# Optimization experiments

Hardware: AMD Instinct MI355X
Metric: run time of the kernel (lower is better)

## Reference

```python
import jax, jax.numpy as jnp
import numpy as np

D_MODEL = 1024
NUM_HEADS = 16
MAX_LEN = 512  # chunk_size
BATCH = 2
SEQ_LEN = 2048


def _mha(x, w_in, b_in, w_out, b_out, num_heads):
    """torch.nn.MultiheadAttention (eval mode, self-attn) over the last-but-one axis.
    x: (..., S, d). Packed in-proj weight w_in: (3d, d), out-proj w_out: (d, d)."""
    *batch, S, d = x.shape
    hd = d // num_heads
    qkv = x @ w_in.T + b_in                      # (..., S, 3d)
    q, k, v = jnp.split(qkv, 3, axis=-1)
    def heads(t):
        return t.reshape(*batch, S, num_heads, hd)
    q, k, v = heads(q), heads(k), heads(v)
    scale = 1.0 / np.sqrt(hd).astype(np.float32)
    scores = jnp.einsum('...qhd,...khd->...hqk', q, k) * scale
    attn = jax.nn.softmax(scores, axis=-1)
    o = jnp.einsum('...hqk,...khd->...qhd', attn, v).reshape(*batch, S, d)
    return o @ w_out.T + b_out


def setup_inputs() -> dict:
    key = jax.random.key(0)
    ks = jax.random.split(key, 5)
    d = D_MODEL
    s = 0.02
    return {
        'x': jax.random.normal(ks[0], (BATCH, SEQ_LEN, d), dtype=jnp.float32),
        'w_in_l': jax.random.normal(ks[1], (3 * d, d), dtype=jnp.float32) * s,
        'b_in_l': jnp.zeros((3 * d,), jnp.float32),
        'w_out_l': jax.random.normal(ks[2], (d, d), dtype=jnp.float32) * s,
        'b_out_l': jnp.zeros((d,), jnp.float32),
        'w_in_g': jax.random.normal(ks[3], (3 * d, d), dtype=jnp.float32) * s,
        'b_in_g': jnp.zeros((3 * d,), jnp.float32),
        'w_out_g': jax.random.normal(ks[4], (d, d), dtype=jnp.float32) * s,
        'b_out_g': jnp.zeros((d,), jnp.float32),
    }


def reference(x, w_in_l, b_in_l, w_out_l, b_out_l, w_in_g, b_in_g, w_out_g, b_out_g):
    B, S, d = x.shape
    cs = MAX_LEN
    nc = S // cs
    # (B, nc, cs, d) -> (B, cs, nc, d): for each intra-chunk position, attend across chunks.
    xc = x.reshape(B, nc, cs, d).transpose(0, 2, 1, 3)
    # Vectorized replacement for the python loop over chunk positions:
    # batched MHA with batch (B, cs) and sequence length nc.
    loc = _mha(xc, w_in_l, b_in_l, w_out_l, b_out_l, NUM_HEADS)  # (B, cs, nc, d)
    # Faithful to torch: stack -> (nc, cs, B, d), transpose(1,2) -> (nc, B, cs, d),
    # then raw reshape to (B, S, d) (a layout-reinterpreting view, preserved here).
    loc = loc.transpose(2, 0, 1, 3).reshape(B, S, d)
    # Global full self-attention over the whole sequence.
    return _mha(loc, w_in_g, b_in_g, w_out_g, b_out_g, NUM_HEADS)
```

## Files before the change

kernel.cpp:

```cpp
#include <hip/hip_runtime.h>

#define BB 2
#define SS 2048
#define DD 1024
#define HH 16
#define HD 64
#define CS 512
#define NC 4
#define TD 3072
#define MM 4096

typedef __attribute__((ext_vector_type(8))) short short8;
typedef __attribute__((ext_vector_type(4))) float floatx4;

__device__ __forceinline__ float bf2f(unsigned short h) {
  union { unsigned int u; float f; } v; v.u = ((unsigned int)h) << 16; return v.f;
}
__device__ __forceinline__ unsigned short f2bf(float f) {
  union { float f; unsigned int u; } v; v.f = f;
  unsigned int r = (v.u + 0x7fffu + ((v.u >> 16) & 1u)) >> 16;
  return (unsigned short)r;
}
__device__ __forceinline__ short8 ld8f(const float* p) {
  floatx4 f0 = *(const floatx4*)p;
  floatx4 f1 = *(const floatx4*)(p + 4);
  short8 o;
  o[0] = (short)f2bf(f0[0]); o[1] = (short)f2bf(f0[1]);
  o[2] = (short)f2bf(f0[2]); o[3] = (short)f2bf(f0[3]);
  o[4] = (short)f2bf(f1[0]); o[5] = (short)f2bf(f1[1]);
  o[6] = (short)f2bf(f1[2]); o[7] = (short)f2bf(f1[3]);
  return o;
}
__device__ __forceinline__ short8 scale8_eighth(short8 a) {
  short8 o;
#pragma unroll
  for (int j = 0; j < 8; ++j) o[j] = (short)f2bf(bf2f((unsigned short)a[j]) * 0.125f);
  return o;
}
__device__ __forceinline__ void async16(const void* g, void* l) {
  __builtin_amdgcn_global_load_lds((const __attribute__((address_space(1))) void*)g,
                                   (__attribute__((address_space(3))) void*)l, 16, 0, 0);
}

__global__ __launch_bounds__(256) void cvt_bf16(const float* __restrict__ in,
                                                unsigned short* __restrict__ out, int n) {
  int i = (blockIdx.x * 256 + threadIdx.x) * 8;
  if (i < n) *(short8*)(out + i) = ld8f(in + i);
}

template <int W_F32, int C_F32>
__global__ __launch_bounds__(256) void gemm_bt_bias(
    const unsigned short* __restrict__ A, const void* __restrict__ Wv,
    const float* __restrict__ bias, void* __restrict__ Cv, int M, int N, int K) {
  __shared__ unsigned short sA[128 * 32];
  __shared__ unsigned short sB[128 * 32];
  const int tid = threadIdx.x;
  const int wid = tid >> 6, lane = tid & 63;
  const int quad = lane >> 4, l15 = lane & 15;
  const int wm = wid & 1, wn = wid >> 1;
  const int bm = blockIdx.y, bn = blockIdx.x;

  floatx4 acc[4][4];
#pragma unroll
  for (int i = 0; i < 4; ++i)
#pragma unroll
    for (int j = 0; j < 4; ++j) acc[i][j] = (floatx4){0.f, 0.f, 0.f, 0.f};

  const int r = tid >> 2;
  const int kc = (tid & 3) * 8;
  const unsigned short* gA = A + (size_t)(bm * 128 + r) * K + kc;
  const float*          gWf = (const float*)Wv          + (size_t)(bn * 128 + r) * K + kc;
  const unsigned short* gWh = (const unsigned short*)Wv + (size_t)(bn * 128 + r) * K + kc;
  unsigned short* lA = sA + wid * 512;
  unsigned short* lB = sB + wid * 512;

  for (int k0 = 0; k0 < K; k0 += 32) {
    async16(gA + k0, lA);
    async16(gA + (size_t)64 * K + k0, lA + 2048);
    if (W_F32) {
      short8 b0 = ld8f(gWf + k0);
      short8 b1 = ld8f(gWf + (size_t)64 * K + k0);
      *(short8*)(sB + r * 32 + kc) = b0;
      *(short8*)(sB + (64 + r) * 32 + kc) = b1;
    } else {
      async16(gWh + k0, lB);
      async16(gWh + (size_t)64 * K + k0, lB + 2048);
    }
    __syncthreads();

    short8 af[4], bfr[4];
#pragma unroll
    for (int i = 0; i < 4; ++i)
      af[i] = *(const short8*)(sA + (wm * 64 + i * 16 + l15) * 32 + quad * 8);
#pragma unroll
    for (int j = 0; j < 4; ++j)
      bfr[j] = *(const short8*)(sB + (wn * 64 + j * 16 + l15) * 32 + quad * 8);
#pragma unroll
    for (int i = 0; i < 4; ++i)
#pragma unroll
      for (int j = 0; j < 4; ++j)
        acc[i][j] = __builtin_amdgcn_mfma_f32_16x16x32_bf16(af[i], bfr[j], acc[i][j], 0, 0, 0);
    __syncthreads();
  }

#pragma unroll
  for (int j = 0; j < 4; ++j) {
    int n = bn * 128 + wn * 64 + j * 16 + l15;
    float bv = bias[n];
#pragma unroll
    for (int i = 0; i < 4; ++i) {
      int mrow = bm * 128 + wm * 64 + i * 16 + quad * 4;
#pragma unroll
      for (int rr = 0; rr < 4; ++rr) {
        float v = acc[i][j][rr] + bv;
        if (C_F32) ((float*)Cv)[(size_t)(mrow + rr) * N + n] = v;
        else ((unsigned short*)Cv)[(size_t)(mrow + rr) * N + n] = f2bf(v);
      }
    }
  }
}

__global__ __launch_bounds__(256) void attn_local(const unsigned short* __restrict__ QKV,
                                                  unsigned short* __restrict__ O) {
  const int tid = threadIdx.x;
  const int wid = tid >> 6, lane = tid & 63;
  const int idx = blockIdx.x * 4 + wid;
  const int h = idx & 15, c = (idx >> 4) & 511, b = idx >> 13;

  float q[NC], k[NC], v[NC];
#pragma unroll
  for (int n = 0; n < NC; ++n) {
    size_t base = (size_t)(b * SS + n * CS + c) * TD + h * HD + lane;
    q[n] = bf2f(QKV[base]);
    k[n] = bf2f(QKV[base + DD]);
    v[n] = bf2f(QKV[base + 2 * DD]);
  }
  float s[NC][NC];
#pragma unroll
  for (int m = 0; m < NC; ++m)
#pragma unroll
    for (int n = 0; n < NC; ++n) {
      float p = q[m] * k[n];
#pragma unroll
      for (int off = 32; off >= 1; off >>= 1) p += __shfl_xor(p, off);
      s[m][n] = p * 0.125f;
    }
#pragma unroll
  for (int m = 0; m < NC; ++m) {
    float mx = fmaxf(fmaxf(s[m][0], s[m][1]), fmaxf(s[m][2], s[m][3]));
    float e[NC], sum = 0.f;
#pragma unroll
    for (int n = 0; n < NC; ++n) { e[n] = __expf(s[m][n] - mx); sum += e[n]; }
    float o = (e[0] * v[0] + e[1] * v[1] + e[2] * v[2] + e[3] * v[3]) / sum;
    O[(size_t)(m * (BB * CS) + b * CS + c) * DD + h * HD + lane] = f2bf(o);
  }
}

__global__ __launch_bounds__(256) void transpose_v(const unsigned short* __restrict__ QKV,
                                                   unsigned short* __restrict__ VT) {
  __shared__ unsigned short sT[64 * 64];
  const int tid = threadIdx.x;
  const int bh = blockIdx.x, b = bh >> 4, h = bh & 15;
  const int s0 = blockIdx.y * 64;
#pragma unroll
  for (int it = 0; it < 2; ++it) {
    int C = it * 256 + tid;
    int t = C >> 3, dc = C & 7;
    short8 v = *(const short8*)(QKV + (size_t)(b * SS + s0 + t) * TD + 2 * DD + h * HD + dc * 8);
    *(short8*)(sT + t * 64 + ((dc ^ (t & 7)) << 3)) = v;
  }
  __syncthreads();
#pragma unroll
  for (int it = 0; it < 2; ++it) {
    int C = it * 256 + tid;
    int d = C >> 3, tc = C & 7;
    short8 o;
#pragma unroll
    for (int j = 0; j < 8; ++j) {
      int t = tc * 8 + j;
      o[j] = (short)sT[t * 64 + (((d >> 3) ^ (t & 7)) << 3) + (d & 7)];
    }
    *(short8*)(VT + ((size_t)(bh * 64 + d)) * SS + s0 + tc * 8) = o;
  }
}

__global__ __launch_bounds__(256) void attn_global(
    const unsigned short* __restrict__ Q, const unsigned short* __restrict__ K,
    const unsigned short* __restrict__ VT, unsigned short* __restrict__ O) {
  __shared__ unsigned short sK[64 * 64];
  __shared__ unsigned short sVT[64 * 64];
  __shared__ unsigned short sP[4][16 * 64];
  const int tid = threadIdx.x;
  const int wid = tid >> 6, lane = tid & 63;
  const int quad = lane >> 4, l15 = lane & 15;
  const int bh = blockIdx.x;
  const int b = bh >> 4, h = bh & 15;
  const int q0 = blockIdx.y * 64 + wid * 16;

  const unsigned short* qrow = Q + (size_t)(b * SS + q0 + l15) * TD + h * HD + quad * 8;
  const short8 qf0 = scale8_eighth(*(const short8*)(qrow));
  const short8 qf1 = scale8_eighth(*(const short8*)(qrow + 32));

  float lsum[4] = {0.f, 0.f, 0.f, 0.f};
  floatx4 oacc[4];
#pragma unroll
  for (int s = 0; s < 4; ++s) oacc[s] = (floatx4){0.f, 0.f, 0.f, 0.f};

  unsigned short* myP = &sP[wid][0];

  for (int kt = 0; kt < SS / 64; ++kt) {
    const int kbase = kt * 64;
#pragma unroll
    for (int it = 0; it < 2; ++it) {
      int P = it * 256 + tid;
      int key = P >> 3, dc = P & 7;
      short8 kv = *(const short8*)(K + (size_t)(b * SS + kbase + key) * TD + h * HD + dc * 8);
      *(short8*)(sK + key * 64 + ((dc ^ (key & 7)) << 3)) = kv;
    }
#pragma unroll
    for (int it = 0; it < 2; ++it) {
      int P = it * 256 + tid;
      int dim = P >> 3, kcc = P & 7;
      short8 vv = *(const short8*)(VT + ((size_t)(bh * 64 + dim)) * SS + kbase + kcc * 8);
      *(short8*)(sVT + dim * 64 + ((kcc ^ (dim & 7)) << 3)) = vv;
    }
    __syncthreads();

    floatx4 sacc[4];
#pragma unroll
    for (int sub = 0; sub < 4; ++sub) {
      int key = sub * 16 + l15;
      int c0 = (quad ^ (key & 7)) << 3;
      short8 kf0 = *(const short8*)(sK + key * 64 + c0);
      short8 kf1 = *(const short8*)(sK + key * 64 + (c0 ^ 32));
      floatx4 z = (floatx4){0.f, 0.f, 0.f, 0.f};
      z = __builtin_amdgcn_mfma_f32_16x16x32_bf16(qf0, kf0, z, 0, 0, 0);
      z = __builtin_amdgcn_mfma_f32_16x16x32_bf16(qf1, kf1, z, 0, 0, 0);
      sacc[sub] = z;
    }

#pragma unroll
    for (int sub = 0; sub < 4; ++sub) {
      int key = sub * 16 + l15;
      int kc8 = key >> 3, k7 = key & 7;
#pragma unroll
      for (int rr = 0; rr < 4; ++rr) {
        float e = __expf(fminf(sacc[sub][rr], 60.f));
        lsum[rr] += e;
        int m = quad * 4 + rr;
        myP[m * 64 + ((kc8 ^ (m & 7)) << 3) + k7] = f2bf(e);
      }
    }
    __asm__ volatile("s_waitcnt lgkmcnt(0)" ::: "memory");
    {
      int c0 = (quad ^ (l15 & 7)) << 3;
      short8 pf0 = *(const short8*)(myP + l15 * 64 + c0);
      short8 pf1 = *(const short8*)(myP + l15 * 64 + (c0 ^ 32));
#pragma unroll
      for (int sub = 0; sub < 4; ++sub) {
        int n = sub * 16 + l15;
        int v0 = (quad ^ (n & 7)) << 3;
        short8 vt0 = *(const short8*)(sVT + n * 64 + v0);
        short8 vt1 = *(const short8*)(sVT + n * 64 + (v0 ^ 32));
        oacc[sub] = __builtin_amdgcn_mfma_f32_16x16x32_bf16(pf0, vt0, oacc[sub], 0, 0, 0);
        oacc[sub] = __builtin_amdgcn_mfma_f32_16x16x32_bf16(pf1, vt1, oacc[sub], 0, 0, 0);
      }
    }
    __syncthreads();
  }

  float linv[4];
#pragma unroll
  for (int rr = 0; rr < 4; ++rr) {
    float t = lsum[rr];
#pragma unroll
    for (int off = 8; off >= 1; off >>= 1) t += __shfl_xor(t, off);
    linv[rr] = 1.f / t;
  }
#pragma unroll
  for (int sub = 0; sub < 4; ++sub)
#pragma unroll
    for (int rr = 0; rr < 4; ++rr) {
      int m = quad * 4 + rr;
      int row = b * SS + q0 + m;
      O[(size_t)row * DD + h * HD + sub * 16 + l15] = f2bf(oacc[sub][rr] * linv[rr]);
    }
}

extern "C" void kernel_launch(void* const* d_in, const int* in_sizes, int n_in,
                              void* d_out, int out_size, void* d_ws, size_t ws_size,
                              hipStream_t stream) {
  const float* x       = (const float*)d_in[0];
  const float* w_in_l  = (const float*)d_in[1];
  const float* b_in_l  = (const float*)d_in[2];
  const float* w_out_l = (const float*)d_in[3];
  const float* b_out_l = (const float*)d_in[4];
  const float* w_in_g  = (const float*)d_in[5];
  const float* b_in_g  = (const float*)d_in[6];
  const float* w_out_g = (const float*)d_in[7];
  const float* b_out_g = (const float*)d_in[8];

  unsigned short* wsA = (unsigned short*)d_ws;
  unsigned short* wsB = wsA + (size_t)MM * TD;
  unsigned short* dob = (unsigned short*)d_out;
  unsigned short* wbf_out_l = dob;
  unsigned short* wbf_in_g  = dob + (size_t)DD * DD;
  unsigned short* wbf_in_l  = dob + 4 * (size_t)DD * DD;
  unsigned short* o1        = dob + 4 * (size_t)DD * DD;
  unsigned short* vtbuf     = dob;

  dim3 blk(256);
  cvt_bf16<<<dim3(DD * DD / 2048), blk, 0, stream>>>(w_out_l, wbf_out_l, DD * DD);
  cvt_bf16<<<dim3(TD * DD / 2048), blk, 0, stream>>>(w_in_g, wbf_in_g, TD * DD);
  cvt_bf16<<<dim3(TD * DD / 2048), blk, 0, stream>>>(w_in_l, wbf_in_l, TD * DD);
  cvt_bf16<<<dim3(MM * DD / 2048), blk, 0, stream>>>(x, wsB, MM * DD);

  gemm_bt_bias<0, 0><<<dim3(TD / 128, MM / 128), blk, 0, stream>>>(wsB, wbf_in_l, b_in_l, wsA, MM, TD, DD);
  attn_local<<<dim3(BB * CS * HH / 4), blk, 0, stream>>>(wsA, o1);
  gemm_bt_bias<0, 0><<<dim3(DD / 128, MM / 128), blk, 0, stream>>>(o1, wbf_out_l, b_out_l, wsB, MM, DD, DD);
  gemm_bt_bias<0, 0><<<dim3(TD / 128, MM / 128), blk, 0, stream>>>(wsB, wbf_in_g, b_in_g, wsA, MM, TD, DD);
  transpose_v<<<dim3(BB * HH, SS / 64), blk, 0, stream>>>(wsA, vtbuf);
  attn_global<<<dim3(BB * HH, SS / 64), blk, 0, stream>>>(wsA, wsA + DD, vtbuf, wsB);
  gemm_bt_bias<1, 1><<<dim3(DD / 128, MM / 128), blk, 0, stream>>>(wsB, w_out_g, b_out_g, d_out, MM, DD, DD);
}
```

Before: 336.8 us.

## Drop LDS staging in global attention and give each wave two query tiles

The global attention kernel no longer stages K and V^T tiles in shared memory with block barriers. Each wave now reads K and V fragments straight from global memory and reuses them across two 16-row query groups, so each block covers 128 queries. The softmax probability is truncated to bf16 by bit masking, which also drops the exp clamp. The final output projection weights are converted to bf16 first so the last GEMM runs in its bf16-weight variant. The risks are more uncoalesced global and L2 traffic, higher register pressure, half as many blocks, and no overflow guard on exp.

```diff
diff --git a/kernel.cpp b/kernel.cpp
--- a/kernel.cpp
+++ b/kernel.cpp
@@ -185,106 +185,112 @@
 }
 
 __global__ __launch_bounds__(256) void attn_global(
-    const unsigned short* __restrict__ Q, const unsigned short* __restrict__ K,
+    const unsigned short* __restrict__ Q, const unsigned short* __restrict__ Kp,
     const unsigned short* __restrict__ VT, unsigned short* __restrict__ O) {
-  __shared__ unsigned short sK[64 * 64];
-  __shared__ unsigned short sVT[64 * 64];
-  __shared__ unsigned short sP[4][16 * 64];
+  __shared__ unsigned short sP[4][32 * 64];
   const int tid = threadIdx.x;
   const int wid = tid >> 6, lane = tid & 63;
   const int quad = lane >> 4, l15 = lane & 15;
   const int bh = blockIdx.x;
   const int b = bh >> 4, h = bh & 15;
-  const int q0 = blockIdx.y * 64 + wid * 16;
-
-  const unsigned short* qrow = Q + (size_t)(b * SS + q0 + l15) * TD + h * HD + quad * 8;
-  const short8 qf0 = scale8_eighth(*(const short8*)(qrow));
-  const short8 qf1 = scale8_eighth(*(const short8*)(qrow + 32));
-
-  float lsum[4] = {0.f, 0.f, 0.f, 0.f};
-  floatx4 oacc[4];
-#pragma unroll
-  for (int s = 0; s < 4; ++s) oacc[s] = (floatx4){0.f, 0.f, 0.f, 0.f};
+  const int q0 = blockIdx.y * 128 + wid * 32;
+
+  short8 qf[2][2];
+#pragma unroll
+  for (int g = 0; g < 2; ++g) {
+    const unsigned short* qr = Q + (size_t)(b * SS + q0 + g * 16 + l15) * TD + h * HD + quad * 8;
+    qf[g][0] = scale8_eighth(*(const short8*)qr);
+    qf[g][1] = scale8_eighth(*(const short8*)(qr + 32));
+  }
+
+  float lsum[2][4];
+  floatx4 oacc[2][4];
+#pragma unroll
+  for (int g = 0; g < 2; ++g)
+#pragma unroll
+    for (int s = 0; s < 4; ++s) { lsum[g][s] = 0.f; oacc[g][s] = (floatx4){0.f, 0.f, 0.f, 0.f}; }
 
   unsigned short* myP = &sP[wid][0];
+  const unsigned short* vbase = VT + (size_t)(bh * 64) * SS;
 
   for (int kt = 0; kt < SS / 64; ++kt) {
     const int kbase = kt * 64;
-#pragma unroll
-    for (int it = 0; it < 2; ++it) {
-      int P = it * 256 + tid;
-      int key = P >> 3, dc = P & 7;
-      short8 kv = *(const short8*)(K + (size_t)(b * SS + kbase + key) * TD + h * HD + dc * 8);
-      *(short8*)(sK + key * 64 + ((dc ^ (key & 7)) << 3)) = kv;
-    }
-#pragma unroll
-    for (int it = 0; it < 2; ++it) {
-      int P = it * 256 + tid;
-      int dim = P >> 3, kcc = P & 7;
-      short8 vv = *(const short8*)(VT + ((size_t)(bh * 64 + dim)) * SS + kbase + kcc * 8);
-      *(short8*)(sVT + dim * 64 + ((kcc ^ (dim & 7)) << 3)) = vv;
-    }
-    __syncthreads();
-
-    floatx4 sacc[4];
+
+    floatx4 sacc[2][4];
 #pragma unroll
     for (int sub = 0; sub < 4; ++sub) {
       int key = sub * 16 + l15;
-      int c0 = (quad ^ (key & 7)) << 3;
-      short8 kf0 = *(const short8*)(sK + key * 64 + c0);
-      short8 kf1 = *(const short8*)(sK + key * 64 + (c0 ^ 32));
-      floatx4 z = (floatx4){0.f, 0.f, 0.f, 0.f};
-      z = __builtin_amdgcn_mfma_f32_16x16x32_bf16(qf0, kf0, z, 0, 0, 0);
-      z = __builtin_amdgcn_mfma_f32_16x16x32_bf16(qf1, kf1, z, 0, 0, 0);
-      sacc[sub] = z;
+      const unsigned short* kr = Kp + (size_t)(b * SS + kbase + key) * TD + h * HD + quad * 8;
+      short8 kf0 = *(const short8*)kr;
+      short8 kf1 = *(const short8*)(kr + 32);
+#pragma unroll
+      for (int g = 0; g < 2; ++g) {
+        floatx4 z = (floatx4){0.f, 0.f, 0.f, 0.f};
+        z = __builtin_amdgcn_mfma_f32_16x16x32_bf16(qf[g][0], kf0, z, 0, 0, 0);
+        z = __builtin_amdgcn_mfma_f32_16x16x32_bf16(qf[g][1], kf1, z, 0, 0, 0);
+        sacc[g][sub] = z;
+      }
+    }
+
+#pragma unroll
+    for (int g = 0; g < 2; ++g)
+#pragma unroll
+      for (int sub = 0; sub < 4; ++sub) {
+        int kc8 = sub * 2 + (l15 >> 3), k7 = l15 & 7;
+#pragma unroll
+        for (int rr = 0; rr < 4; ++rr) {
+          unsigned int u = __float_as_uint(__expf(sacc[g][sub][rr]));
+          lsum[g][rr] += __uint_as_float(u & 0xffff0000u);
+          int row = g * 16 + quad * 4 + rr;
+          myP[row * 64 + (((kc8 ^ (row & 7) ^ ((row >> 3) << 1))) << 3) + k7] =
+              (unsigned short)(u >> 16);
+        }
+      }
+    __asm__ volatile("s_waitcnt lgkmcnt(0)" ::: "memory");
+
+    short8 pf[2][2];
+#pragma unroll
+    for (int g = 0; g < 2; ++g) {
+      int row = g * 16 + l15;
+      int sw = (row & 7) ^ ((row >> 3) << 1);
+#pragma unroll
+      for (int c = 0; c < 2; ++c)
+        pf[g][c] = *(const short8*)(myP + row * 64 + (((c * 4 + quad) ^ sw) << 3));
     }
 
 #pragma unroll
     for (int sub = 0; sub < 4; ++sub) {
-      int key = sub * 16 + l15;
-      int kc8 = key >> 3, k7 = key & 7;
+      int n = sub * 16 + l15;
+      const unsigned short* vr = vbase + (size_t)n * SS + kbase + quad * 8;
+      short8 vt0 = *(const short8*)vr;
+      short8 vt1 = *(const short8*)(vr + 32);
+#pragma unroll
+      for (int g = 0; g < 2; ++g) {
+        oacc[g][sub] = __builtin_amdgcn_mfma_f32_16x16x32_bf16(pf[g][0], vt0, oacc[g][sub], 0, 0, 0);
+        oacc[g][sub] = __builtin_amdgcn_mfma_f32_16x16x32_bf16(pf[g][1], vt1, oacc[g][sub], 0, 0, 0);
+      }
+    }
+  }
+
+  float linv[2][4];
+#pragma unroll
+  for (int g = 0; g < 2; ++g)
+#pragma unroll
+    for (int rr = 0; rr < 4; ++rr) {
+      float t = lsum[g][rr];
+#pragma unroll
+      for (int off = 8; off >= 1; off >>= 1) t += __shfl_xor(t, off);
+      linv[g][rr] = 1.f / t;
+    }
+#pragma unroll
+  for (int g = 0; g < 2; ++g)
+#pragma unroll
+    for (int sub = 0; sub < 4; ++sub)
 #pragma unroll
       for (int rr = 0; rr < 4; ++rr) {
-        float e = __expf(fminf(sacc[sub][rr], 60.f));
-        lsum[rr] += e;
-        int m = quad * 4 + rr;
-        myP[m * 64 + ((kc8 ^ (m & 7)) << 3) + k7] = f2bf(e);
-      }
-    }
-    __asm__ volatile("s_waitcnt lgkmcnt(0)" ::: "memory");
-    {
-      int c0 = (quad ^ (l15 & 7)) << 3;
-      short8 pf0 = *(const short8*)(myP + l15 * 64 + c0);
-      short8 pf1 = *(const short8*)(myP + l15 * 64 + (c0 ^ 32));
-#pragma unroll
-      for (int sub = 0; sub < 4; ++sub) {
-        int n = sub * 16 + l15;
-        int v0 = (quad ^ (n & 7)) << 3;
-        short8 vt0 = *(const short8*)(sVT + n * 64 + v0);
-        short8 vt1 = *(const short8*)(sVT + n * 64 + (v0 ^ 32));
-        oacc[sub] = __builtin_amdgcn_mfma_f32_16x16x32_bf16(pf0, vt0, oacc[sub], 0, 0, 0);
-        oacc[sub] = __builtin_amdgcn_mfma_f32_16x16x32_bf16(pf1, vt1, oacc[sub], 0, 0, 0);
-      }
-    }
-    __syncthreads();
-  }
-
-  float linv[4];
-#pragma unroll
-  for (int rr = 0; rr < 4; ++rr) {
-    float t = lsum[rr];
-#pragma unroll
-    for (int off = 8; off >= 1; off >>= 1) t += __shfl_xor(t, off);
-    linv[rr] = 1.f / t;
-  }
-#pragma unroll
-  for (int sub = 0; sub < 4; ++sub)
-#pragma unroll
-    for (int rr = 0; rr < 4; ++rr) {
-      int m = quad * 4 + rr;
-      int row = b * SS + q0 + m;
-      O[(size_t)row * DD + h * HD + sub * 16 + l15] = f2bf(oacc[sub][rr] * linv[rr]);
-    }
+        int row = b * SS + q0 + g * 16 + quad * 4 + rr;
+        O[(size_t)row * DD + h * HD + sub * 16 + l15] = f2bf(oacc[g][sub][rr] * linv[g][rr]);
+      }
 }
 
 extern "C" void kernel_launch(void* const* d_in, const int* in_sizes, int n_in,
@@ -320,6 +326,7 @@
   gemm_bt_bias<0, 0><<<dim3(DD / 128, MM / 128), blk, 0, stream>>>(o1, wbf_out_l, b_out_l, wsB, MM, DD, DD);
   gemm_bt_bias<0, 0><<<dim3(TD / 128, MM / 128), blk, 0, stream>>>(wsB, wbf_in_g, b_in_g, wsA, MM, TD, DD);
   transpose_v<<<dim3(BB * HH, SS / 64), blk, 0, stream>>>(wsA, vtbuf);
-  attn_global<<<dim3(BB * HH, SS / 64), blk, 0, stream>>>(wsA, wsA + DD, vtbuf, wsB);
-  gemm_bt_bias<1, 1><<<dim3(DD / 128, MM / 128), blk, 0, stream>>>(wsB, w_out_g, b_out_g, d_out, MM, DD, DD);
-}
+  attn_global<<<dim3(BB * HH, SS / 128), blk, 0, stream>>>(wsA, wsA + DD, vtbuf, wsB);
+  cvt_bf16<<<dim3(DD * DD / 2048), blk, 0, stream>>>(w_out_g, wsA, DD * DD);
+  gemm_bt_bias<0, 1><<<dim3(DD / 128, MM / 128), blk, 0, stream>>>(wsB, wsA, b_out_g, d_out, MM, DD, DD);
+}
```

Result: slower. 386.0 us (+14.6%).
